# Kernel optimization log

Hardware: AMD Instinct MI355X
Metric: run time of the kernel (lower is better)

Reference implementation:

```python
import jax, jax.numpy as jnp
import numpy as np

B, H, L, DK = 8, 8, 512, 64
LK, C = 512, 5


def setup_inputs() -> dict:
    key = jax.random.key(0)
    ks = jax.random.split(key, 6)
    d_in = LK * H * DK  # l_k * d_model
    return {
        "Q": jax.random.normal(ks[0], (B, H, L, DK), dtype=jnp.float32),
        "K": jax.random.normal(ks[1], (B, H, LK, DK), dtype=jnp.float32),
        # scale by 1/sqrt(fan_in) so softmax inputs are sane
        "W_proj": jax.random.normal(ks[2], (d_in, C), dtype=jnp.float32) / np.sqrt(d_in),
        "b_proj": jnp.zeros((C,), dtype=jnp.float32),
        "W_q": jax.random.normal(ks[3], (C, C), dtype=jnp.float32) / np.sqrt(C),
        "b_q": jnp.zeros((C,), dtype=jnp.float32),
        "W_k": jax.random.normal(ks[4], (C, C), dtype=jnp.float32) / np.sqrt(C),
        "b_k": jnp.zeros((C,), dtype=jnp.float32),
    }


def reference(Q, K, W_proj, b_proj, W_q, b_q, W_k, b_k):
    b, h, l, d_k = Q.shape
    l_k = K.shape[2]
    n_clusters = b_proj.shape[0]
    hd = h * d_k

    # cluster projections over flattened K
    ck_proj = K.reshape(b, -1) @ W_proj + b_proj            # (b, C)
    cluster_q = jax.nn.softmax(ck_proj @ W_q + b_q, axis=-1)  # (b, C)
    cluster_k = jax.nn.softmax(ck_proj @ W_k + b_k, axis=-1)  # (b, C)

    # Gaussian likelihood term (torch.std is unbiased -> ddof=1)
    mu = jnp.mean(cluster_q, axis=0)                         # (C,)
    sigma = jax.nn.softplus(jnp.std(cluster_k, axis=0, ddof=1))
    log_prob = (-0.5 * ((cluster_k - mu) / sigma) ** 2
                - jnp.log(sigma) - 0.5 * jnp.log(2.0 * jnp.pi))
    # CrossEntropyLoss with prob targets: mean_b(-sum target*log_softmax(input))
    ce = jnp.mean(-jnp.sum(cluster_q * jax.nn.log_softmax(cluster_q, axis=-1), axis=-1))
    loss = -jnp.mean(log_prob) + ce

    # cluster assignment per batch element
    inds = jnp.argmax(cluster_q, axis=-1)                    # (b,) in [0, C)

    # The original per-cluster loop with where(K_cluster != i+1, K_inds, 0) then
    # mean(dim=0)[0] reduces to: mean over batch of K_re[:,0,:] masked where
    # assignment != i+1, broadcast across l_k.
    K_re = K.reshape(b, l_k, hd)
    row0 = K_re[:, 0, :]                                     # (b, hd)
    keep = (inds[None, :] != (jnp.arange(n_clusters) + 1)[:, None]).astype(Q.dtype)  # (C, b)
    means = (keep @ row0) / b                                # (C, hd)

    # broadcast to (b, C, l_k, hd) then raw reshape to (b, h, C, l_k, d_k)
    cm = jnp.broadcast_to(means[None, :, None, :], (b, n_clusters, l_k, hd))
    cm = cm.reshape(b, h, n_clusters, l_k, d_k)

    scale = 1.0 / np.sqrt(d_k)
    scores_qk = jnp.einsum('bhqd,bhkd->bhqk', Q, K) * scale          # (b,h,l,l_k)
    scores_qc = jnp.einsum('bhqd,bhckd->bhcqk', Q, cm) * scale       # (b,h,C,l,l_k)
    # max over cat([qk, qc], dim=2) == elementwise max of qk and max_c qc
    final_score = jnp.maximum(scores_qk, jnp.max(scores_qc, axis=2))
    return final_score, loss
```

## Files before the change

### kernel.cpp

```cpp
#include <hip/hip_runtime.h>
#include <math.h>

#define NB 8
#define NH 8
#define SEQ 512
#define DK 64
#define NC 5
#define D_IN 262144
#define OUT_SCORE (NB*NH*SEQ*SEQ)
#define PROJ_BLOCKS 128

typedef short short8 __attribute__((ext_vector_type(8)));
typedef float f32x16 __attribute__((ext_vector_type(16)));

__device__ __forceinline__ short8 pack8(float4 a, float4 b) {
  union { short8 s; unsigned u[4]; } r;
  asm("v_cvt_pk_bf16_f32 %0, %1, %2" : "=v"(r.u[0]) : "v"(a.x), "v"(a.y));
  asm("v_cvt_pk_bf16_f32 %0, %1, %2" : "=v"(r.u[1]) : "v"(a.z), "v"(a.w));
  asm("v_cvt_pk_bf16_f32 %0, %1, %2" : "=v"(r.u[2]) : "v"(b.x), "v"(b.y));
  asm("v_cvt_pk_bf16_f32 %0, %1, %2" : "=v"(r.u[3]) : "v"(b.z), "v"(b.w));
  return r.s;
}

__global__ __launch_bounds__(256) void proj_kernel(const float* __restrict__ K,
                                                   const float* __restrict__ Wp,
                                                   float* __restrict__ part) {
  const float4* Wp4 = (const float4*)Wp;
  float acc[NB][NC];
#pragma unroll
  for (int b = 0; b < NB; ++b)
#pragma unroll
    for (int c = 0; c < NC; ++c) acc[b][c] = 0.f;

#pragma unroll
  for (int it = 0; it < 2; ++it) {
    int i4 = blockIdx.x * 512 + it * 256 + threadIdx.x;
    float w[20];
#pragma unroll
    for (int t = 0; t < 5; ++t) {
      float4 v = Wp4[i4 * 5 + t];
      w[4*t+0] = v.x; w[4*t+1] = v.y; w[4*t+2] = v.z; w[4*t+3] = v.w;
    }
#pragma unroll
    for (int b = 0; b < NB; ++b) {
      float4 kv = ((const float4*)(K + (size_t)b * D_IN))[i4];
      float ke[4] = {kv.x, kv.y, kv.z, kv.w};
#pragma unroll
      for (int e = 0; e < 4; ++e)
#pragma unroll
        for (int c = 0; c < NC; ++c)
          acc[b][c] = fmaf(ke[e], w[5*e + c], acc[b][c]);
    }
  }

  __shared__ float red[4][NB * NC];
  int wave = threadIdx.x >> 6;
  int lane = threadIdx.x & 63;
#pragma unroll
  for (int bc = 0; bc < NB * NC; ++bc) {
    float v = acc[bc / NC][bc % NC];
#pragma unroll
    for (int off = 32; off > 0; off >>= 1) v += __shfl_down(v, off);
    if (lane == 0) red[wave][bc] = v;
  }
  __syncthreads();
  if (threadIdx.x < NB * NC)
    part[threadIdx.x * PROJ_BLOCKS + blockIdx.x] =
        red[0][threadIdx.x] + red[1][threadIdx.x] +
        red[2][threadIdx.x] + red[3][threadIdx.x];
}

#define LDSTRIDE 72
__global__ __launch_bounds__(256) void score_kernel(
    const float* __restrict__ Q, const float* __restrict__ K,
    const float* __restrict__ part, const float* __restrict__ bp,
    const float* __restrict__ Wq, const float* __restrict__ bq,
    const float* __restrict__ Wk, const float* __restrict__ bk,
    float* __restrict__ out) {
  __shared__ short Qs[128 * LDSTRIDE];
  __shared__ short Ks[64 * LDSTRIDE];
  __shared__ __align__(16) float sp[1280];
  float* means_sh = sp;
  int*   inds_sh  = (int*)&sp[1024];
  float* cs4      = &sp[1032];
  float* cq_sh    = &sp[1192];
  float* ckk_sh   = &sp[1232];
  float* ce_sh    = &sp[1272];

  const int bh   = blockIdx.x;
  const int qblk = blockIdx.y << 7;
  const int kblk = blockIdx.z << 6;
  const int h  = bh & 7;
  const int tid = threadIdx.x;
  const int w = tid >> 6, lane = tid & 63;
  const int lo5 = lane & 31, hi = lane >> 5;
  const int wq = w << 5;

  const float* Qg = Q + (size_t)bh * (SEQ * DK) + (size_t)qblk * DK;
  const float* Kg = K + (size_t)bh * (SEQ * DK) + (size_t)kblk * DK;

#pragma unroll
  for (int i = 0; i < 4; ++i) {
    int f8 = i * 256 + tid;
    int row = f8 >> 3, c8 = f8 & 7;
    const float4* qp = (const float4*)(Qg + row * DK + c8 * 8);
    *(short8*)&Qs[row * LDSTRIDE + c8 * 8] = pack8(qp[0], qp[1]);
  }
#pragma unroll
  for (int i = 0; i < 2; ++i) {
    int f8 = i * 256 + tid;
    int row = f8 >> 3, c8 = f8 & 7;
    const float4* kp = (const float4*)(Kg + row * DK + c8 * 8);
    *(short8*)&Ks[row * LDSTRIDE + c8 * 8] = pack8(kp[0], kp[1]);
  }

  if (tid < 160) {
    int col = tid >> 2, sub = tid & 3;
    const float4* p4 = (const float4*)part + col * 32 + sub * 8;
    float4 s4 = {0.f, 0.f, 0.f, 0.f};
#pragma unroll
    for (int i = 0; i < 8; ++i) {
      float4 v = p4[i];
      s4.x += v.x; s4.y += v.y; s4.z += v.z; s4.w += v.w;
    }
    cs4[sub * 40 + col] = (s4.x + s4.y) + (s4.z + s4.w);
  }
  __syncthreads();
  if (tid < 40)
    cs4[tid] = cs4[tid] + cs4[40 + tid] + cs4[80 + tid] + cs4[120 + tid];
  __syncthreads();
  if (tid < NB) {
    float cp[NC], zq[NC], zk[NC];
#pragma unroll
    for (int c = 0; c < NC; ++c) cp[c] = cs4[tid * NC + c] + bp[c];
#pragma unroll
    for (int c = 0; c < NC; ++c) { zq[c] = bq[c]; zk[c] = bk[c]; }
#pragma unroll
    for (int j = 0; j < NC; ++j)
#pragma unroll
      for (int c = 0; c < NC; ++c) {
        zq[c] = fmaf(cp[j], Wq[j * NC + c], zq[c]);
        zk[c] = fmaf(cp[j], Wk[j * NC + c], zk[c]);
      }
    float m = zq[0];
#pragma unroll
    for (int c = 1; c < NC; ++c) m = fmaxf(m, zq[c]);
    float e[NC], s = 0.f;
#pragma unroll
    for (int c = 0; c < NC; ++c) { e[c] = expf(zq[c] - m); s += e[c]; }
    float inv = 1.f / s;
    float p[NC];
#pragma unroll
    for (int c = 0; c < NC; ++c) { p[c] = e[c] * inv; cq_sh[tid * NC + c] = p[c]; }
    int am = 0; float bv = p[0];
#pragma unroll
    for (int c = 1; c < NC; ++c) if (p[c] > bv) { bv = p[c]; am = c; }
    inds_sh[tid] = am;
    float se = 0.f;
#pragma unroll
    for (int c = 0; c < NC; ++c) se += expf(p[c] - bv);
    float lse = bv + logf(se);
    float ceb = 0.f;
#pragma unroll
    for (int c = 0; c < NC; ++c) ceb -= p[c] * (p[c] - lse);
    ce_sh[tid] = ceb;
    m = zk[0];
#pragma unroll
    for (int c = 1; c < NC; ++c) m = fmaxf(m, zk[c]);
    s = 0.f;
#pragma unroll
    for (int c = 0; c < NC; ++c) { e[c] = expf(zk[c] - m); s += e[c]; }
    inv = 1.f / s;
#pragma unroll
    for (int c = 0; c < NC; ++c) ckk_sh[tid * NC + c] = e[c] * inv;
  }
  __syncthreads();

  if (blockIdx.x == 0 && blockIdx.y == 0 && blockIdx.z == 0 && tid == 0) {
    float mu[NC];
#pragma unroll
    for (int c = 0; c < NC; ++c) {
      float sm = 0.f;
      for (int b = 0; b < NB; ++b) sm += cq_sh[b * NC + c];
      mu[c] = sm * 0.125f;
    }
    float loss_lp = 0.f;
#pragma unroll
    for (int c = 0; c < NC; ++c) {
      float sm = 0.f;
      for (int b = 0; b < NB; ++b) sm += ckk_sh[b * NC + c];
      float mk = sm * 0.125f;
      float var = 0.f;
      for (int b = 0; b < NB; ++b) {
        float d = ckk_sh[b * NC + c] - mk;
        var += d * d;
      }
      var *= (1.f / 7.f);
      float sd = sqrtf(var);
      float sigma = log1pf(expf(sd));
      float ls = logf(sigma);
      for (int b = 0; b < NB; ++b) {
        float z = (ckk_sh[b * NC + c] - mu[c]) / sigma;
        loss_lp += -0.5f * z * z - ls - 0.91893853320467274f;
      }
    }
    float ce = 0.f;
    for (int b = 0; b < NB; ++b) ce += ce_sh[b];
    ce *= 0.125f;
    out[OUT_SCORE] = -(loss_lp / 40.f) + ce;
  }

  const int cmin = (5 * h) >> 3;
  const int cmax = (5 * h + 4) >> 3;
  {
    int c2 = tid >> 7;
    int c  = c2 ? cmax : cmin;
    int j4 = (tid & 127) << 2;
    float4 sm = {0.f, 0.f, 0.f, 0.f};
#pragma unroll
    for (int b = 0; b < NB; ++b) {
      if (inds_sh[b] != c + 1) {
        float4 kv = *(const float4*)(K + (size_t)b * D_IN + j4);
        sm.x += kv.x; sm.y += kv.y; sm.z += kv.z; sm.w += kv.w;
      }
    }
    sm.x *= 0.125f; sm.y *= 0.125f; sm.z *= 0.125f; sm.w *= 0.125f;
    *(float4*)&means_sh[c2 * 512 + j4] = sm;
  }
  __syncthreads();

  short8 mfrag[4];
#pragma unroll
  for (int s = 0; s < 4; ++s) {
    float4 a = {0.f, 0.f, 0.f, 0.f}, b = {0.f, 0.f, 0.f, 0.f};
    if (lo5 < 16) {
      const float* mp = means_sh + (lo5 >> 3 << 9) + (lo5 & 7) * 64 + s * 16 + hi * 8;
      a = *(const float4*)mp;
      b = *(const float4*)(mp + 4);
    }
    mfrag[s] = pack8(a, b);
  }

  __syncthreads();

  f32x16 zero;
#pragma unroll
  for (int x = 0; x < 16; ++x) zero[x] = 0.f;

  f32x16 acc0 = zero, acc1 = zero, aq = zero;
#pragma unroll
  for (int s = 0; s < 4; ++s) {
    int co = s * 16 + hi * 8;
    short8 a  = *(const short8*)&Qs[(wq + lo5)  * LDSTRIDE + co];
    short8 b0 = *(const short8*)&Ks[lo5         * LDSTRIDE + co];
    short8 b1 = *(const short8*)&Ks[(32 + lo5)  * LDSTRIDE + co];
    acc0 = __builtin_amdgcn_mfma_f32_32x32x16_bf16(a, b0, acc0, 0, 0, 0);
    acc1 = __builtin_amdgcn_mfma_f32_32x32x16_bf16(a, b1, acc1, 0, 0, 0);
    aq   = __builtin_amdgcn_mfma_f32_32x32x16_bf16(mfrag[s], a, aq, 0, 0, 0);
  }

  float* qcbuf = sp;
  {
    int qb = w * 320 + lo5 * 10 + 4 * hi;
    float2 p;
    p.x = fmaxf(aq[0], aq[4]) * 0.125f;
    p.y = fmaxf(aq[1], aq[5]) * 0.125f;
    *(float2*)&qcbuf[qb] = p;
    p.x = fmaxf(aq[2], aq[6]) * 0.125f;
    p.y = fmaxf(aq[3], aq[7]) * 0.125f;
    *(float2*)&qcbuf[qb + 2] = p;
  }

  float* ob = out + (size_t)bh * (SEQ * SEQ);
  const int kc0 = kblk + lo5;
  const int r = lo5 & 7;
  const int qcb = w * 320 + r;
#pragma unroll
  for (int g = 0; g < 4; ++g) {
#pragma unroll
    for (int e = 0; e < 4; ++e) {
      int reg = 4 * g + e;
      int ql = e + 8 * g + 4 * hi;
      float qc = qcbuf[qcb + ql * 10];
      int qrow = qblk + wq + ql;
      ob[(size_t)qrow * SEQ + kc0]      = fmaxf(acc0[reg] * 0.125f, qc);
      ob[(size_t)qrow * SEQ + kc0 + 32] = fmaxf(acc1[reg] * 0.125f, qc);
    }
  }
}

extern "C" void kernel_launch(void* const* d_in, const int* in_sizes, int n_in,
                              void* d_out, int out_size, void* d_ws, size_t ws_size,
                              hipStream_t stream) {
  const float* Q  = (const float*)d_in[0];
  const float* K  = (const float*)d_in[1];
  const float* Wp = (const float*)d_in[2];
  const float* bp = (const float*)d_in[3];
  const float* Wq = (const float*)d_in[4];
  const float* bq = (const float*)d_in[5];
  const float* Wk = (const float*)d_in[6];
  const float* bk = (const float*)d_in[7];
  float* out = (float*)d_out;

  float* part = (float*)d_ws;

  proj_kernel<<<PROJ_BLOCKS, 256, 0, stream>>>(K, Wp, part);
  score_kernel<<<dim3(64, 4, 8), 256, 0, stream>>>(Q, K, part, bp, Wq, bq, Wk, bk, out);
}
```

Measured before the change: 124.9 us.

## Process two 64-key tiles per block with prefetched second K tile

Each score block now covers 128 key columns instead of 64, halving the grid along the key dimension. The second K tile is loaded into registers early and packed into shared memory after the first tile's output is written. The Q tile load, the cluster/softmax prologue and the Q-times-cluster-mean max are then computed once per 128 keys instead of once per 64, cutting redundant per-block setup. In exchange there are fewer blocks (1024), more register pressure from the prefetch buffer and second accumulators, and two extra barriers.

```diff
diff --git a/kernel.cpp b/kernel.cpp
--- a/kernel.cpp
+++ b/kernel.cpp
@@ -87,9 +87,9 @@
   float* ckk_sh   = &sp[1232];
   float* ce_sh    = &sp[1272];
 
-  const int bh   = blockIdx.x;
-  const int qblk = blockIdx.y << 7;
-  const int kblk = blockIdx.z << 6;
+  const int bh    = blockIdx.x;
+  const int qblk  = blockIdx.y << 7;
+  const int kbase = blockIdx.z << 7;
   const int h  = bh & 7;
   const int tid = threadIdx.x;
   const int w = tid >> 6, lane = tid & 63;
@@ -97,7 +97,7 @@
   const int wq = w << 5;
 
   const float* Qg = Q + (size_t)bh * (SEQ * DK) + (size_t)qblk * DK;
-  const float* Kg = K + (size_t)bh * (SEQ * DK) + (size_t)kblk * DK;
+  const float* Kg = K + (size_t)bh * (SEQ * DK) + (size_t)kbase * DK;
 
 #pragma unroll
   for (int i = 0; i < 4; ++i) {
@@ -112,6 +112,15 @@
     int row = f8 >> 3, c8 = f8 & 7;
     const float4* kp = (const float4*)(Kg + row * DK + c8 * 8);
     *(short8*)&Ks[row * LDSTRIDE + c8 * 8] = pack8(kp[0], kp[1]);
+  }
+  float4 kpre[4];
+#pragma unroll
+  for (int i = 0; i < 2; ++i) {
+    int f8 = i * 256 + tid;
+    int row = f8 >> 3, c8 = f8 & 7;
+    const float4* kp = (const float4*)(Kg + (64 + row) * DK + c8 * 8);
+    kpre[2*i]   = kp[0];
+    kpre[2*i+1] = kp[1];
   }
 
   if (tid < 160) {
@@ -272,7 +281,7 @@
   }
 
   float* ob = out + (size_t)bh * (SEQ * SEQ);
-  const int kc0 = kblk + lo5;
+  const int kc0 = kbase + lo5;
   const int r = lo5 & 7;
   const int qcb = w * 320 + r;
 #pragma unroll
@@ -285,6 +294,38 @@
       int qrow = qblk + wq + ql;
       ob[(size_t)qrow * SEQ + kc0]      = fmaxf(acc0[reg] * 0.125f, qc);
       ob[(size_t)qrow * SEQ + kc0 + 32] = fmaxf(acc1[reg] * 0.125f, qc);
+    }
+  }
+
+  __syncthreads();
+#pragma unroll
+  for (int i = 0; i < 2; ++i) {
+    int f8 = i * 256 + tid;
+    int row = f8 >> 3, c8 = f8 & 7;
+    *(short8*)&Ks[row * LDSTRIDE + c8 * 8] = pack8(kpre[2*i], kpre[2*i+1]);
+  }
+  __syncthreads();
+
+  f32x16 acc0b = zero, acc1b = zero;
+#pragma unroll
+  for (int s = 0; s < 4; ++s) {
+    int co = s * 16 + hi * 8;
+    short8 a  = *(const short8*)&Qs[(wq + lo5)  * LDSTRIDE + co];
+    short8 b0 = *(const short8*)&Ks[lo5         * LDSTRIDE + co];
+    short8 b1 = *(const short8*)&Ks[(32 + lo5)  * LDSTRIDE + co];
+    acc0b = __builtin_amdgcn_mfma_f32_32x32x16_bf16(a, b0, acc0b, 0, 0, 0);
+    acc1b = __builtin_amdgcn_mfma_f32_32x32x16_bf16(a, b1, acc1b, 0, 0, 0);
+  }
+#pragma unroll
+  for (int g = 0; g < 4; ++g) {
+#pragma unroll
+    for (int e = 0; e < 4; ++e) {
+      int reg = 4 * g + e;
+      int ql = e + 8 * g + 4 * hi;
+      float qc = qcbuf[qcb + ql * 10];
+      int qrow = qblk + wq + ql;
+      ob[(size_t)qrow * SEQ + kc0 + 64] = fmaxf(acc0b[reg] * 0.125f, qc);
+      ob[(size_t)qrow * SEQ + kc0 + 96] = fmaxf(acc1b[reg] * 0.125f, qc);
     }
   }
 }
@@ -305,5 +346,5 @@
   float* part = (float*)d_ws;
 
   proj_kernel<<<PROJ_BLOCKS, 256, 0, stream>>>(K, Wp, part);
-  score_kernel<<<dim3(64, 4, 8), 256, 0, stream>>>(Q, K, part, bp, Wq, bq, Wk, bk, out);
+  score_kernel<<<dim3(64, 4, 4), 256, 0, stream>>>(Q, K, part, bp, Wq, bq, Wk, bk, out);
 }
```

Measured after the change: 119.6 us. 1.04x faster.
